# Optimization experiments

Hardware: AMD Instinct MI355X
Metric: run time of the kernel (lower is better)

## Reference

```python
import jax, jax.numpy as jnp
import numpy as np

FEAT_DIM = 1024
NUM_HEADS = 16
HEAD_DIM = FEAT_DIM // NUM_HEADS
B, T = 8, 1024


def setup_inputs() -> dict:
    key = jax.random.key(0)
    k_x, k_wqkv, k_bqkv, k_wp, k_bp = jax.random.split(key, 5)
    s = 1.0 / np.sqrt(FEAT_DIM)
    return {
        "x": jax.random.normal(k_x, (B, T, FEAT_DIM), dtype=jnp.float32),
        "padding_mask": jnp.zeros((B, T), dtype=bool),  # True = padded position
        "W_qkv": jax.random.normal(k_wqkv, (3 * FEAT_DIM, FEAT_DIM), dtype=jnp.float32) * s,
        "b_qkv": jax.random.normal(k_bqkv, (3 * FEAT_DIM,), dtype=jnp.float32) * 0.01,
        "W_proj": jax.random.normal(k_wp, (FEAT_DIM, FEAT_DIM), dtype=jnp.float32) * s,
        "b_proj": jax.random.normal(k_bp, (FEAT_DIM,), dtype=jnp.float32) * 0.01,
        "scale_factor": jnp.asarray(1.0 / np.sqrt(HEAD_DIM), dtype=jnp.float32),
    }


def reference(x, padding_mask, W_qkv, b_qkv, W_proj, b_proj, scale_factor):
    Bb, Tt, D = x.shape
    H, hd = NUM_HEADS, HEAD_DIM
    # fused QKV projection: [B,T,3D] -> [3,B,H,T,hd]
    qkv = (x @ W_qkv.T + b_qkv).reshape(Bb, Tt, 3, H, hd).transpose(2, 0, 3, 1, 4)
    q, k, v = qkv[0], qkv[1], qkv[2]
    # scores [B,H,T,T]
    attn = jnp.einsum("bhqd,bhkd->bhqk", q, k) * scale_factor
    causal = jnp.triu(jnp.ones((Tt, Tt), dtype=bool), k=1)  # [T,T]
    mask = causal[None, None] | padding_mask[:, None, None, :]  # [B,H,T,T] via broadcast
    attn = jnp.where(mask, -jnp.inf, attn)
    attn = jax.nn.softmax(attn, axis=-1)
    # dropout is identity in eval mode
    out = jnp.einsum("bhqk,bhkd->bqhd", attn, v).reshape(Bb, Tt, D)
    return out @ W_proj.T + b_proj
```

## Files before the change

### kernel.cpp

```cpp
#include <hip/hip_runtime.h>
#include <cstdint>
#include <cstddef>

typedef unsigned short u16;
typedef __attribute__((ext_vector_type(2))) unsigned short u16x2;
typedef __attribute__((ext_vector_type(4))) unsigned short u16x4;
typedef __attribute__((ext_vector_type(8))) unsigned short u16x8;
typedef __attribute__((ext_vector_type(8))) short s16x8;
typedef __attribute__((ext_vector_type(4))) float f32x4;

__device__ __forceinline__ u16 f2bf(float f) {
  uint32_t u = __float_as_uint(f);
  u += 0x7fffu + ((u >> 16) & 1u);
  return (u16)(u >> 16);
}

__device__ __forceinline__ f32x4 mfma16(s16x8 a, s16x8 b, f32x4 c) {
  return __builtin_amdgcn_mfma_f32_16x16x32_bf16(a, b, c, 0, 0, 0);
}

#define GLDS16(gp, lp) __builtin_amdgcn_global_load_lds(                     \
    (const __attribute__((address_space(1))) void*)(gp),                      \
    (__attribute__((address_space(3))) void*)(lp), 16, 0, 0)

__global__ void cvt_all(const float* __restrict__ x, const float* __restrict__ wq,
                        const float* __restrict__ wp, u16* __restrict__ xb,
                        u16* __restrict__ wqb, u16* __restrict__ wpb) {
  const int n4x = 2097152, n4q = 786432, n4p = 262144;
  const int total = n4x + n4q + n4p;
  const int stride = gridDim.x * blockDim.x;
  for (int i = blockIdx.x * blockDim.x + threadIdx.x; i < total; i += stride) {
    const float* src;
    u16* dst;
    int j = i;
    if (j < n4x) {
      src = x; dst = xb;
    } else if (j < n4x + n4q) {
      j -= n4x; src = wq; dst = wqb;
    } else {
      j -= n4x + n4q; src = wp; dst = wpb;
    }
    f32x4 v = ((const f32x4*)src)[j];
    u16x4 o;
    o[0] = f2bf(v[0]); o[1] = f2bf(v[1]); o[2] = f2bf(v[2]); o[3] = f2bf(v[3]);
    ((u16x4*)dst)[j] = o;
  }
}

template <int OUT_BF16>
__global__ __launch_bounds__(256, 2)
void gemm_bt(const u16* __restrict__ A, const u16* __restrict__ B,
             const float* __restrict__ bias, u16* __restrict__ Cb,
             float* __restrict__ Cf, int M, int N, int K, int tilesN) {
  __shared__ u16 lA[128 * 32];
  __shared__ u16 lB[128 * 32];

  int bid = blockIdx.x;
  int cpx = gridDim.x >> 3;
  bid = (bid & 7) * cpx + (bid >> 3);

  const int tm = bid / tilesN, tn = bid % tilesN;
  const int row0 = tm * 128, col0 = tn * 128;
  const int tid = threadIdx.x;
  const int lane = tid & 63, wave = tid >> 6;

  const u16* Ag = A + (size_t)(row0 + (tid >> 2)) * K + (tid & 3) * 8;
  const u16* Bg = B + (size_t)(col0 + (tid >> 2)) * K + (tid & 3) * 8;
  const int ldsoff = tid * 8;

  const int wm = (wave >> 1) * 64, wn = (wave & 1) * 64;
  const int fr = lane & 15, fk = (lane >> 4) * 8;

  f32x4 acc[4][4] = {};

  for (int k0 = 0; k0 < K; k0 += 32) {
    __syncthreads();
    GLDS16(Ag + k0, &lA[ldsoff]);
    GLDS16(Ag + (size_t)64 * K + k0, &lA[2048 + ldsoff]);
    GLDS16(Bg + k0, &lB[ldsoff]);
    GLDS16(Bg + (size_t)64 * K + k0, &lB[2048 + ldsoff]);
    __syncthreads();

    s16x8 af[4], bfr[4];
#pragma unroll
    for (int i = 0; i < 4; ++i) af[i] = *(const s16x8*)&lA[(wm + i * 16 + fr) * 32 + fk];
#pragma unroll
    for (int i = 0; i < 4; ++i) bfr[i] = *(const s16x8*)&lB[(wn + i * 16 + fr) * 32 + fk];
#pragma unroll
    for (int i = 0; i < 4; ++i)
#pragma unroll
      for (int j = 0; j < 4; ++j) acc[i][j] = mfma16(af[i], bfr[j], acc[i][j]);
  }

#pragma unroll
  for (int i = 0; i < 4; ++i) {
#pragma unroll
    for (int r = 0; r < 4; ++r) {
      const int row = row0 + wm + i * 16 + (lane >> 4) * 4 + r;
#pragma unroll
      for (int j = 0; j < 4; ++j) {
        const int col = col0 + wn + j * 16 + fr;
        const float v = acc[i][j][r] + bias[col];
        if (OUT_BF16)
          Cb[(size_t)row * N + col] = f2bf(v);
        else
          Cf[(size_t)row * N + col] = v;
      }
    }
  }
}

__global__ __launch_bounds__(256)
void vtrans(const u16* __restrict__ qkv, u16* __restrict__ vt) {
  __shared__ u16 lT[64][68];
  const int bid = blockIdx.x;
  const int bh = bid >> 4;
  const int tt = bid & 15;
  const int b = bh >> 4, h = bh & 15;
  const int tid = threadIdx.x;
  const int row = tid >> 2;
  const int cc = (tid & 3) * 16;

  const u16* src = qkv + (size_t)(b * 1024 + tt * 64 + row) * 3072 + 2048 + h * 64 + cc;
  *(u16x8*)&lT[row][cc] = *(const u16x8*)src;
  *(u16x8*)&lT[row][cc + 8] = *(const u16x8*)(src + 8);
  __syncthreads();

  u16 tmp[16];
#pragma unroll
  for (int i = 0; i < 16; ++i) tmp[i] = lT[cc + i][row];
  u16* dst = vt + (size_t)(bh * 64 + row) * 1024 + tt * 64 + cc;
  *(u16x8*)dst = *(u16x8*)&tmp[0];
  *(u16x8*)(dst + 8) = *(u16x8*)&tmp[8];
}

template <int NF, bool CAUSAL>
__device__ __forceinline__ void attn_step(
    const u16* __restrict__ Kbase, const u16* __restrict__ Vbase,
    const float* __restrict__ pb, u16* __restrict__ lp, int kvb, int qb,
    int fr, int grp, const s16x8 qf[2][2], f32x4 oacc[2][4], float m2[2],
    float l2[2], float cs) {
  f32x4 st[NF][2];
#pragma unroll
  for (int f = 0; f < NF; ++f) {
    const u16* kp = Kbase + (size_t)(kvb + f * 16 + fr) * 3072 + grp * 8;
    s16x8 ka0 = *(const s16x8*)kp;
    s16x8 ka1 = *(const s16x8*)(kp + 32);
    f32x4 a0 = {0.f, 0.f, 0.f, 0.f}, a1 = {0.f, 0.f, 0.f, 0.f};
    a0 = mfma16(ka0, qf[0][0], a0);
    a0 = mfma16(ka1, qf[0][1], a0);
    a1 = mfma16(ka0, qf[1][0], a1);
    a1 = mfma16(ka1, qf[1][1], a1);
    st[f][0] = a0;
    st[f][1] = a1;
  }

  f32x4 pbv[NF];
#pragma unroll
  for (int f = 0; f < NF; ++f)
    pbv[f] = *(const f32x4*)&pb[kvb + f * 16 + grp * 4];

  float tm[2];
#pragma unroll
  for (int g = 0; g < 2; ++g) {
    const int q = qb + g * 16 + fr;
    float t = -3.0e38f;
#pragma unroll
    for (int f = 0; f < NF; ++f)
#pragma unroll
      for (int r = 0; r < 4; ++r) {
        float v = __builtin_fmaf(st[f][g][r], cs, pbv[f][r]);
        if (CAUSAL) {
          const int kv = kvb + f * 16 + grp * 4 + r;
          v = (kv > q) ? -3.0e38f : v;
        }
        st[f][g][r] = v;
        t = fmaxf(t, v);
      }
    t = fmaxf(t, __shfl_xor(t, 16));
    t = fmaxf(t, __shfl_xor(t, 32));
    tm[g] = t;
  }

  const bool defer = __all((tm[0] <= m2[0] + 8.0f) && (tm[1] <= m2[1] + 8.0f)) != 0;
  if (!defer) {
#pragma unroll
    for (int g = 0; g < 2; ++g) {
      const float mn = fmaxf(m2[g], tm[g]);
      const float al = __expf(m2[g] - mn);
      m2[g] = mn;
      l2[g] *= al;
      float ar[4];
#pragma unroll
      for (int r = 0; r < 4; ++r) ar[r] = __shfl(al, grp * 4 + r);
#pragma unroll
      for (int nf = 0; nf < 4; ++nf) {
        oacc[g][nf][0] *= ar[0];
        oacc[g][nf][1] *= ar[1];
        oacc[g][nf][2] *= ar[2];
        oacc[g][nf][3] *= ar[3];
      }
    }
  }

#pragma unroll
  for (int g = 0; g < 2; ++g) {
    float rsum = 0.f;
#pragma unroll
    for (int f = 0; f < NF; ++f)
#pragma unroll
      for (int rp = 0; rp < 2; ++rp) {
        const float p0 = __expf(st[f][g][2 * rp] - m2[g]);
        const float p1 = __expf(st[f][g][2 * rp + 1] - m2[g]);
        rsum += p0 + p1;
        const uint32_t pk = __builtin_amdgcn_perm(
            __float_as_uint(p1) + 0x8000u, __float_as_uint(p0) + 0x8000u,
            0x07060302u);
        *(uint32_t*)&lp[(g * 16 + fr) * 72 + f * 16 + grp * 4 + 2 * rp] = pk;
      }
    rsum += __shfl_xor(rsum, 16);
    rsum += __shfl_xor(rsum, 32);
    l2[g] += rsum;
  }

  s16x8 pa[2][NF / 2];
#pragma unroll
  for (int g = 0; g < 2; ++g)
#pragma unroll
    for (int kc = 0; kc < NF / 2; ++kc)
      pa[g][kc] = *(const s16x8*)&lp[(g * 16 + fr) * 72 + kc * 32 + grp * 8];
#pragma unroll
  for (int nf = 0; nf < 4; ++nf) {
    const u16* vp = Vbase + (size_t)(nf * 16 + fr) * 1024 + kvb + grp * 8;
    s16x8 vb0 = *(const s16x8*)vp;
#pragma unroll
    for (int g = 0; g < 2; ++g) {
      f32x4 o = oacc[g][nf];
      o = mfma16(pa[g][0], vb0, o);
      if (NF == 4) o = mfma16(pa[g][1], *(const s16x8*)(vp + 32), o);
      oacc[g][nf] = o;
    }
  }
}

__global__ __launch_bounds__(256)
void attn3(const u16* __restrict__ qkv, const u16* __restrict__ vt,
           const unsigned char* __restrict__ pmask,
           const float* __restrict__ scale_ptr, u16* __restrict__ outp) {
  __shared__ u16 lP[4][32 * 72];
  __shared__ float lPb[1024];
  const int tid = threadIdx.x;
  const int lane = tid & 63, wave = tid >> 6;
  const int fr = lane & 15, grp = lane >> 4;
  const int w = blockIdx.x * 4 + wave;
  const int qc = 31 - (w >> 7);
  const int bh = w & 127;
  const int b = bh >> 4, h = bh & 15;
  const int qb = qc * 32;
  const float cs = scale_ptr[0];

  for (int i = tid; i < 1024; i += 256)
    lPb[i] = pmask[b * 1024 + i] ? -3.0e38f : 0.0f;
  __syncthreads();

  const u16* Kbase = qkv + (size_t)b * 1024 * 3072 + 1024 + h * 64;
  const u16* Vbase = vt + (size_t)bh * 64 * 1024;
  u16* lp = &lP[wave][0];

  s16x8 qf[2][2];
#pragma unroll
  for (int g = 0; g < 2; ++g)
#pragma unroll
    for (int c = 0; c < 2; ++c)
      qf[g][c] = *(const s16x8*)(qkv + (size_t)(b * 1024 + qb + g * 16 + fr) * 3072 +
                                 h * 64 + c * 32 + grp * 8);

  f32x4 oacc[2][4] = {};
  float m2[2] = {-1e30f, -1e30f};
  float l2[2] = {0.0f, 0.0f};

  const int FT = qc >> 1;
  for (int t = 0; t < FT; ++t)
    attn_step<4, false>(Kbase, Vbase, lPb, lp, t * 64, qb, fr, grp, qf, oacc, m2, l2, cs);
  if (qc & 1)
    attn_step<2, false>(Kbase, Vbase, lPb, lp, qb - 32, qb, fr, grp, qf, oacc, m2, l2, cs);
  attn_step<2, true>(Kbase, Vbase, lPb, lp, qb, qb, fr, grp, qf, oacc, m2, l2, cs);

#pragma unroll
  for (int g = 0; g < 2; ++g) {
    float linv[4];
#pragma unroll
    for (int r = 0; r < 4; ++r) linv[r] = 1.0f / __shfl(l2[g], grp * 4 + r);
#pragma unroll
    for (int nf = 0; nf < 4; ++nf)
#pragma unroll
      for (int r = 0; r < 4; ++r) {
        const int tq = qb + g * 16 + grp * 4 + r;
        outp[(size_t)(b * 1024 + tq) * 1024 + h * 64 + nf * 16 + fr] =
            f2bf(oacc[g][nf][r] * linv[r]);
      }
  }
}

extern "C" void kernel_launch(void* const* d_in, const int* in_sizes, int n_in,
                              void* d_out, int out_size, void* d_ws, size_t ws_size,
                              hipStream_t stream) {
  const float* x = (const float*)d_in[0];
  const unsigned char* pmask = (const unsigned char*)d_in[1];
  const float* Wqkv = (const float*)d_in[2];
  const float* bqkv = (const float*)d_in[3];
  const float* Wproj = (const float*)d_in[4];
  const float* bproj = (const float*)d_in[5];
  const float* scale = (const float*)d_in[6];
  float* out = (float*)d_out;

  char* ws = (char*)d_ws;
  u16* xb     = (u16*)(ws + 0);
  u16* vtb    = (u16*)(ws + 0);
  u16* wqkvb  = (u16*)(ws + 16777216);
  u16* wprojb = (u16*)(ws + 23068672);
  u16* qkv    = (u16*)(ws + 25165824);
  u16* attno  = (u16*)(ws + 75497472);
  if (ws_size < (size_t)92274688) return;

  cvt_all<<<2048, 256, 0, stream>>>(x, Wqkv, Wproj, xb, wqkvb, wprojb);

  gemm_bt<1><<<64 * 24, 256, 0, stream>>>(xb, wqkvb, bqkv, qkv, nullptr,
                                          8192, 3072, 1024, 24);
  vtrans<<<2048, 256, 0, stream>>>(qkv, vtb);
  attn3<<<1024, 256, 0, stream>>>(qkv, vtb, pmask, scale, attno);
  gemm_bt<0><<<64 * 8, 256, 0, stream>>>(attno, wprojb, bproj, nullptr, out,
                                         8192, 1024, 1024, 8);
}
```

Before: 266.7 us.

## Shrink attention per-wave query tile to 16 rows and double wave count

The attention kernel now gives each wave 16 query rows instead of 32, launches twice as many blocks, and adds a launch bound of 8 blocks per CU. Register and LDS use per wave drop, which should raise occupancy and give a finer causal-triangle load balance. The cost is that every K/V fragment is now loaded from global memory twice as often per query row, because each wave reuses it across only 16 rows, and the MFMA work per load is halved.

```diff
diff --git a/kernel.cpp b/kernel.cpp
--- a/kernel.cpp
+++ b/kernel.cpp
@@ -135,24 +135,21 @@
 }
 
 template <int NF, bool CAUSAL>
-__device__ __forceinline__ void attn_step(
+__device__ __forceinline__ void attn_step5(
     const u16* __restrict__ Kbase, const u16* __restrict__ Vbase,
     const float* __restrict__ pb, u16* __restrict__ lp, int kvb, int qb,
-    int fr, int grp, const s16x8 qf[2][2], f32x4 oacc[2][4], float m2[2],
-    float l2[2], float cs) {
-  f32x4 st[NF][2];
+    int fr, int grp, const s16x8 qf[2], f32x4 oacc[4], float& m2, float& l2,
+    float cs) {
+  f32x4 st[NF];
 #pragma unroll
   for (int f = 0; f < NF; ++f) {
     const u16* kp = Kbase + (size_t)(kvb + f * 16 + fr) * 3072 + grp * 8;
     s16x8 ka0 = *(const s16x8*)kp;
     s16x8 ka1 = *(const s16x8*)(kp + 32);
-    f32x4 a0 = {0.f, 0.f, 0.f, 0.f}, a1 = {0.f, 0.f, 0.f, 0.f};
-    a0 = mfma16(ka0, qf[0][0], a0);
-    a0 = mfma16(ka1, qf[0][1], a0);
-    a1 = mfma16(ka0, qf[1][0], a1);
-    a1 = mfma16(ka1, qf[1][1], a1);
-    st[f][0] = a0;
-    st[f][1] = a1;
+    f32x4 a = {0.f, 0.f, 0.f, 0.f};
+    a = mfma16(ka0, qf[0], a);
+    a = mfma16(ka1, qf[1], a);
+    st[f] = a;
   }
 
   f32x4 pbv[NF];
@@ -160,103 +157,86 @@
   for (int f = 0; f < NF; ++f)
     pbv[f] = *(const f32x4*)&pb[kvb + f * 16 + grp * 4];
 
-  float tm[2];
-#pragma unroll
-  for (int g = 0; g < 2; ++g) {
-    const int q = qb + g * 16 + fr;
-    float t = -3.0e38f;
-#pragma unroll
-    for (int f = 0; f < NF; ++f)
-#pragma unroll
-      for (int r = 0; r < 4; ++r) {
-        float v = __builtin_fmaf(st[f][g][r], cs, pbv[f][r]);
-        if (CAUSAL) {
-          const int kv = kvb + f * 16 + grp * 4 + r;
-          v = (kv > q) ? -3.0e38f : v;
-        }
-        st[f][g][r] = v;
-        t = fmaxf(t, v);
+  const int q = qb + fr;
+  float t = -3.0e38f;
+#pragma unroll
+  for (int f = 0; f < NF; ++f)
+#pragma unroll
+    for (int r = 0; r < 4; ++r) {
+      float v = __builtin_fmaf(st[f][r], cs, pbv[f][r]);
+      if (CAUSAL) {
+        const int kv = kvb + f * 16 + grp * 4 + r;
+        v = (kv > q) ? -3.0e38f : v;
       }
-    t = fmaxf(t, __shfl_xor(t, 16));
-    t = fmaxf(t, __shfl_xor(t, 32));
-    tm[g] = t;
-  }
-
-  const bool defer = __all((tm[0] <= m2[0] + 8.0f) && (tm[1] <= m2[1] + 8.0f)) != 0;
-  if (!defer) {
-#pragma unroll
-    for (int g = 0; g < 2; ++g) {
-      const float mn = fmaxf(m2[g], tm[g]);
-      const float al = __expf(m2[g] - mn);
-      m2[g] = mn;
-      l2[g] *= al;
-      float ar[4];
-#pragma unroll
-      for (int r = 0; r < 4; ++r) ar[r] = __shfl(al, grp * 4 + r);
-#pragma unroll
-      for (int nf = 0; nf < 4; ++nf) {
-        oacc[g][nf][0] *= ar[0];
-        oacc[g][nf][1] *= ar[1];
-        oacc[g][nf][2] *= ar[2];
-        oacc[g][nf][3] *= ar[3];
-      }
-    }
-  }
-
-#pragma unroll
-  for (int g = 0; g < 2; ++g) {
-    float rsum = 0.f;
-#pragma unroll
-    for (int f = 0; f < NF; ++f)
-#pragma unroll
-      for (int rp = 0; rp < 2; ++rp) {
-        const float p0 = __expf(st[f][g][2 * rp] - m2[g]);
-        const float p1 = __expf(st[f][g][2 * rp + 1] - m2[g]);
-        rsum += p0 + p1;
-        const uint32_t pk = __builtin_amdgcn_perm(
-            __float_as_uint(p1) + 0x8000u, __float_as_uint(p0) + 0x8000u,
-            0x07060302u);
-        *(uint32_t*)&lp[(g * 16 + fr) * 72 + f * 16 + grp * 4 + 2 * rp] = pk;
-      }
-    rsum += __shfl_xor(rsum, 16);
-    rsum += __shfl_xor(rsum, 32);
-    l2[g] += rsum;
-  }
-
-  s16x8 pa[2][NF / 2];
-#pragma unroll
-  for (int g = 0; g < 2; ++g)
-#pragma unroll
-    for (int kc = 0; kc < NF / 2; ++kc)
-      pa[g][kc] = *(const s16x8*)&lp[(g * 16 + fr) * 72 + kc * 32 + grp * 8];
+      st[f][r] = v;
+      t = fmaxf(t, v);
+    }
+  t = fmaxf(t, __shfl_xor(t, 16));
+  t = fmaxf(t, __shfl_xor(t, 32));
+
+  if (!__all(t <= m2 + 8.0f)) {
+    const float mn = fmaxf(m2, t);
+    const float al = __expf(m2 - mn);
+    m2 = mn;
+    l2 *= al;
+    float ar[4];
+#pragma unroll
+    for (int r = 0; r < 4; ++r) ar[r] = __shfl(al, grp * 4 + r);
+#pragma unroll
+    for (int nf = 0; nf < 4; ++nf) {
+      oacc[nf][0] *= ar[0];
+      oacc[nf][1] *= ar[1];
+      oacc[nf][2] *= ar[2];
+      oacc[nf][3] *= ar[3];
+    }
+  }
+
+  float rsum = 0.f;
+#pragma unroll
+  for (int f = 0; f < NF; ++f)
+#pragma unroll
+    for (int rp = 0; rp < 2; ++rp) {
+      const float p0 = __expf(st[f][2 * rp] - m2);
+      const float p1 = __expf(st[f][2 * rp + 1] - m2);
+      rsum += p0 + p1;
+      const uint32_t pk = __builtin_amdgcn_perm(
+          __float_as_uint(p1) + 0x8000u, __float_as_uint(p0) + 0x8000u,
+          0x07060302u);
+      *(uint32_t*)&lp[fr * 72 + f * 16 + grp * 4 + 2 * rp] = pk;
+    }
+  rsum += __shfl_xor(rsum, 16);
+  rsum += __shfl_xor(rsum, 32);
+  l2 += rsum;
+
+  s16x8 pa[NF / 2];
+#pragma unroll
+  for (int kc = 0; kc < NF / 2; ++kc)
+    pa[kc] = *(const s16x8*)&lp[fr * 72 + kc * 32 + grp * 8];
 #pragma unroll
   for (int nf = 0; nf < 4; ++nf) {
     const u16* vp = Vbase + (size_t)(nf * 16 + fr) * 1024 + kvb + grp * 8;
     s16x8 vb0 = *(const s16x8*)vp;
-#pragma unroll
-    for (int g = 0; g < 2; ++g) {
-      f32x4 o = oacc[g][nf];
-      o = mfma16(pa[g][0], vb0, o);
-      if (NF == 4) o = mfma16(pa[g][1], *(const s16x8*)(vp + 32), o);
-      oacc[g][nf] = o;
-    }
-  }
-}
-
-__global__ __launch_bounds__(256)
-void attn3(const u16* __restrict__ qkv, const u16* __restrict__ vt,
+    f32x4 o = oacc[nf];
+    o = mfma16(pa[0], vb0, o);
+    if (NF == 4) o = mfma16(pa[1], *(const s16x8*)(vp + 32), o);
+    oacc[nf] = o;
+  }
+}
+
+__global__ __launch_bounds__(256, 8)
+void attn5(const u16* __restrict__ qkv, const u16* __restrict__ vt,
            const unsigned char* __restrict__ pmask,
            const float* __restrict__ scale_ptr, u16* __restrict__ outp) {
-  __shared__ u16 lP[4][32 * 72];
+  __shared__ u16 lP[4][16 * 72];
   __shared__ float lPb[1024];
   const int tid = threadIdx.x;
   const int lane = tid & 63, wave = tid >> 6;
   const int fr = lane & 15, grp = lane >> 4;
   const int w = blockIdx.x * 4 + wave;
-  const int qc = 31 - (w >> 7);
+  const int qi = 63 - (w >> 7);
   const int bh = w & 127;
   const int b = bh >> 4, h = bh & 15;
-  const int qb = qc * 32;
+  const int qb = qi * 16;
   const float cs = scale_ptr[0];
 
   for (int i = tid; i < 1024; i += 256)
@@ -267,39 +247,34 @@
   const u16* Vbase = vt + (size_t)bh * 64 * 1024;
   u16* lp = &lP[wave][0];
 
-  s16x8 qf[2][2];
-#pragma unroll
-  for (int g = 0; g < 2; ++g)
-#pragma unroll
-    for (int c = 0; c < 2; ++c)
-      qf[g][c] = *(const s16x8*)(qkv + (size_t)(b * 1024 + qb + g * 16 + fr) * 3072 +
-                                 h * 64 + c * 32 + grp * 8);
-
-  f32x4 oacc[2][4] = {};
-  float m2[2] = {-1e30f, -1e30f};
-  float l2[2] = {0.0f, 0.0f};
-
-  const int FT = qc >> 1;
-  for (int t = 0; t < FT; ++t)
-    attn_step<4, false>(Kbase, Vbase, lPb, lp, t * 64, qb, fr, grp, qf, oacc, m2, l2, cs);
-  if (qc & 1)
-    attn_step<2, false>(Kbase, Vbase, lPb, lp, qb - 32, qb, fr, grp, qf, oacc, m2, l2, cs);
-  attn_step<2, true>(Kbase, Vbase, lPb, lp, qb, qb, fr, grp, qf, oacc, m2, l2, cs);
-
-#pragma unroll
-  for (int g = 0; g < 2; ++g) {
-    float linv[4];
-#pragma unroll
-    for (int r = 0; r < 4; ++r) linv[r] = 1.0f / __shfl(l2[g], grp * 4 + r);
-#pragma unroll
-    for (int nf = 0; nf < 4; ++nf)
-#pragma unroll
-      for (int r = 0; r < 4; ++r) {
-        const int tq = qb + g * 16 + grp * 4 + r;
-        outp[(size_t)(b * 1024 + tq) * 1024 + h * 64 + nf * 16 + fr] =
-            f2bf(oacc[g][nf][r] * linv[r]);
-      }
-  }
+  s16x8 qf[2];
+#pragma unroll
+  for (int c = 0; c < 2; ++c)
+    qf[c] = *(const s16x8*)(qkv + (size_t)(b * 1024 + qb + fr) * 3072 +
+                            h * 64 + c * 32 + grp * 8);
+
+  f32x4 oacc[4] = {};
+  float m2 = -1e30f, l2 = 0.0f;
+
+  const int n = qi >> 1;
+  int u = 0;
+  for (; u + 2 <= n; u += 2)
+    attn_step5<4, false>(Kbase, Vbase, lPb, lp, u * 32, qb, fr, grp, qf, oacc, m2, l2, cs);
+  if (u < n)
+    attn_step5<2, false>(Kbase, Vbase, lPb, lp, u * 32, qb, fr, grp, qf, oacc, m2, l2, cs);
+  attn_step5<2, true>(Kbase, Vbase, lPb, lp, n * 32, qb, fr, grp, qf, oacc, m2, l2, cs);
+
+  float linv[4];
+#pragma unroll
+  for (int r = 0; r < 4; ++r) linv[r] = 1.0f / __shfl(l2, grp * 4 + r);
+#pragma unroll
+  for (int nf = 0; nf < 4; ++nf)
+#pragma unroll
+    for (int r = 0; r < 4; ++r) {
+      const int tq = qb + grp * 4 + r;
+      outp[(size_t)(b * 1024 + tq) * 1024 + h * 64 + nf * 16 + fr] =
+          f2bf(oacc[nf][r] * linv[r]);
+    }
 }
 
 extern "C" void kernel_launch(void* const* d_in, const int* in_sizes, int n_in,
@@ -328,7 +303,7 @@
   gemm_bt<1><<<64 * 24, 256, 0, stream>>>(xb, wqkvb, bqkv, qkv, nullptr,
                                           8192, 3072, 1024, 24);
   vtrans<<<2048, 256, 0, stream>>>(qkv, vtb);
-  attn3<<<1024, 256, 0, stream>>>(qkv, vtb, pmask, scale, attno);
+  attn5<<<2048, 256, 0, stream>>>(qkv, vtb, pmask, scale, attno);
   gemm_bt<0><<<64 * 8, 256, 0, stream>>>(attno, wprojb, bproj, nullptr, out,
                                          8192, 1024, 1024, 8);
 }
```

Measured after the change: 364.3 us. 1.37x slower.

## Pair low and high causal query tiles per wave to balance attention work

Applied to the files above, without the earlier changes.

Each wave now processes two 16-row query tiles, one from the start and its mirror from the end of the sequence, so every wave does about the same amount of causal work instead of the old 32-row contiguous blocks of very different length. The key/value loop first runs both tiles together up to the low tile's diagonal, then continues with only the high tile, with the MFMAs, masking and softmax skipped for the inactive tile. Rescale deferral is now decided per tile, and launch bounds ask for 4 blocks per CU. The cost is that K/V fragments loaded in the shared phase feed only 16-row MFMAs, and the template has more variants, which may raise register use.

```diff
diff --git a/kernel.cpp b/kernel.cpp
--- a/kernel.cpp
+++ b/kernel.cpp
@@ -134,25 +134,30 @@
   *(u16x8*)(dst + 8) = *(u16x8*)&tmp[8];
 }
 
-template <int NF, bool CAUSAL>
-__device__ __forceinline__ void attn_step(
+template <int NF, bool LO, bool HI, bool CLO, bool CHI>
+__device__ __forceinline__ void attn_step6(
     const u16* __restrict__ Kbase, const u16* __restrict__ Vbase,
-    const float* __restrict__ pb, u16* __restrict__ lp, int kvb, int qb,
-    int fr, int grp, const s16x8 qf[2][2], f32x4 oacc[2][4], float m2[2],
-    float l2[2], float cs) {
+    const float* __restrict__ pb, u16* __restrict__ lp, int kvb, int qblo,
+    int qbhi, int fr, int grp, const s16x8 qf[2][2], f32x4 oacc[2][4],
+    float m2[2], float l2[2], float cs) {
   f32x4 st[NF][2];
 #pragma unroll
   for (int f = 0; f < NF; ++f) {
     const u16* kp = Kbase + (size_t)(kvb + f * 16 + fr) * 3072 + grp * 8;
     s16x8 ka0 = *(const s16x8*)kp;
     s16x8 ka1 = *(const s16x8*)(kp + 32);
-    f32x4 a0 = {0.f, 0.f, 0.f, 0.f}, a1 = {0.f, 0.f, 0.f, 0.f};
-    a0 = mfma16(ka0, qf[0][0], a0);
-    a0 = mfma16(ka1, qf[0][1], a0);
-    a1 = mfma16(ka0, qf[1][0], a1);
-    a1 = mfma16(ka1, qf[1][1], a1);
-    st[f][0] = a0;
-    st[f][1] = a1;
+    if (LO) {
+      f32x4 a = {0.f, 0.f, 0.f, 0.f};
+      a = mfma16(ka0, qf[0][0], a);
+      a = mfma16(ka1, qf[0][1], a);
+      st[f][0] = a;
+    }
+    if (HI) {
+      f32x4 a = {0.f, 0.f, 0.f, 0.f};
+      a = mfma16(ka0, qf[1][0], a);
+      a = mfma16(ka1, qf[1][1], a);
+      st[f][1] = a;
+    }
   }
 
   f32x4 pbv[NF];
@@ -160,17 +165,18 @@
   for (int f = 0; f < NF; ++f)
     pbv[f] = *(const f32x4*)&pb[kvb + f * 16 + grp * 4];
 
-  float tm[2];
 #pragma unroll
   for (int g = 0; g < 2; ++g) {
-    const int q = qb + g * 16 + fr;
+    if ((g == 0 && !LO) || (g == 1 && !HI)) continue;
+    const bool CG = (g == 0) ? CLO : CHI;
+    const int q = ((g == 0) ? qblo : qbhi) + fr;
     float t = -3.0e38f;
 #pragma unroll
     for (int f = 0; f < NF; ++f)
 #pragma unroll
       for (int r = 0; r < 4; ++r) {
         float v = __builtin_fmaf(st[f][g][r], cs, pbv[f][r]);
-        if (CAUSAL) {
+        if (CG) {
           const int kv = kvb + f * 16 + grp * 4 + r;
           v = (kv > q) ? -3.0e38f : v;
         }
@@ -179,14 +185,9 @@
       }
     t = fmaxf(t, __shfl_xor(t, 16));
     t = fmaxf(t, __shfl_xor(t, 32));
-    tm[g] = t;
-  }
-
-  const bool defer = __all((tm[0] <= m2[0] + 8.0f) && (tm[1] <= m2[1] + 8.0f)) != 0;
-  if (!defer) {
-#pragma unroll
-    for (int g = 0; g < 2; ++g) {
-      const float mn = fmaxf(m2[g], tm[g]);
+
+    if (!__all(t <= m2[g] + 8.0f)) {
+      const float mn = fmaxf(m2[g], t);
       const float al = __expf(m2[g] - mn);
       m2[g] = mn;
       l2[g] *= al;
@@ -201,10 +202,7 @@
         oacc[g][nf][3] *= ar[3];
       }
     }
-  }
-
-#pragma unroll
-  for (int g = 0; g < 2; ++g) {
+
     float rsum = 0.f;
 #pragma unroll
     for (int f = 0; f < NF; ++f)
@@ -225,26 +223,31 @@
 
   s16x8 pa[2][NF / 2];
 #pragma unroll
-  for (int g = 0; g < 2; ++g)
+  for (int g = 0; g < 2; ++g) {
+    if ((g == 0 && !LO) || (g == 1 && !HI)) continue;
 #pragma unroll
     for (int kc = 0; kc < NF / 2; ++kc)
       pa[g][kc] = *(const s16x8*)&lp[(g * 16 + fr) * 72 + kc * 32 + grp * 8];
+  }
 #pragma unroll
   for (int nf = 0; nf < 4; ++nf) {
     const u16* vp = Vbase + (size_t)(nf * 16 + fr) * 1024 + kvb + grp * 8;
     s16x8 vb0 = *(const s16x8*)vp;
+    s16x8 vb1;
+    if (NF == 4) vb1 = *(const s16x8*)(vp + 32);
 #pragma unroll
     for (int g = 0; g < 2; ++g) {
+      if ((g == 0 && !LO) || (g == 1 && !HI)) continue;
       f32x4 o = oacc[g][nf];
       o = mfma16(pa[g][0], vb0, o);
-      if (NF == 4) o = mfma16(pa[g][1], *(const s16x8*)(vp + 32), o);
+      if (NF == 4) o = mfma16(pa[g][1], vb1, o);
       oacc[g][nf] = o;
     }
   }
 }
 
-__global__ __launch_bounds__(256)
-void attn3(const u16* __restrict__ qkv, const u16* __restrict__ vt,
+__global__ __launch_bounds__(256, 4)
+void attn6(const u16* __restrict__ qkv, const u16* __restrict__ vt,
            const unsigned char* __restrict__ pmask,
            const float* __restrict__ scale_ptr, u16* __restrict__ outp) {
   __shared__ u16 lP[4][32 * 72];
@@ -252,11 +255,12 @@
   const int tid = threadIdx.x;
   const int lane = tid & 63, wave = tid >> 6;
   const int fr = lane & 15, grp = lane >> 4;
-  const int w = blockIdx.x * 4 + wave;
-  const int qc = 31 - (w >> 7);
-  const int bh = w & 127;
+  const int bid = blockIdx.x;
+  const int bh = bid & 127;
   const int b = bh >> 4, h = bh & 15;
-  const int qb = qc * 32;
+  const int p = (bid >> 7) * 4 + wave;
+  const int qblo = p * 16;
+  const int qbhi = (63 - p) * 16;
   const float cs = scale_ptr[0];
 
   for (int i = tid; i < 1024; i += 256)
@@ -269,25 +273,47 @@
 
   s16x8 qf[2][2];
 #pragma unroll
-  for (int g = 0; g < 2; ++g)
+  for (int g = 0; g < 2; ++g) {
+    const int qb = g ? qbhi : qblo;
 #pragma unroll
     for (int c = 0; c < 2; ++c)
-      qf[g][c] = *(const s16x8*)(qkv + (size_t)(b * 1024 + qb + g * 16 + fr) * 3072 +
+      qf[g][c] = *(const s16x8*)(qkv + (size_t)(b * 1024 + qb + fr) * 3072 +
                                  h * 64 + c * 32 + grp * 8);
+  }
 
   f32x4 oacc[2][4] = {};
   float m2[2] = {-1e30f, -1e30f};
   float l2[2] = {0.0f, 0.0f};
 
-  const int FT = qc >> 1;
-  for (int t = 0; t < FT; ++t)
-    attn_step<4, false>(Kbase, Vbase, lPb, lp, t * 64, qb, fr, grp, qf, oacc, m2, l2, cs);
-  if (qc & 1)
-    attn_step<2, false>(Kbase, Vbase, lPb, lp, qb - 32, qb, fr, grp, qf, oacc, m2, l2, cs);
-  attn_step<2, true>(Kbase, Vbase, lPb, lp, qb, qb, fr, grp, qf, oacc, m2, l2, cs);
+  const int nlo = (p >> 1) + 1;
+  const int nhi = ((63 - p) >> 1) + 1;
+
+  int u = 0;
+  for (; u + 2 <= nlo - 1; u += 2)
+    attn_step6<4, true, true, false, false>(Kbase, Vbase, lPb, lp, u * 32,
+                                            qblo, qbhi, fr, grp, qf, oacc, m2, l2, cs);
+  if (u < nlo - 1) {
+    attn_step6<2, true, true, false, false>(Kbase, Vbase, lPb, lp, u * 32,
+                                            qblo, qbhi, fr, grp, qf, oacc, m2, l2, cs);
+    ++u;
+  }
+  attn_step6<2, true, true, true, false>(Kbase, Vbase, lPb, lp, (nlo - 1) * 32,
+                                         qblo, qbhi, fr, grp, qf, oacc, m2, l2, cs);
+  u = nlo;
+  for (; u + 2 <= nhi - 1; u += 2)
+    attn_step6<4, false, true, false, false>(Kbase, Vbase, lPb, lp, u * 32,
+                                             qblo, qbhi, fr, grp, qf, oacc, m2, l2, cs);
+  if (u < nhi - 1) {
+    attn_step6<2, false, true, false, false>(Kbase, Vbase, lPb, lp, u * 32,
+                                             qblo, qbhi, fr, grp, qf, oacc, m2, l2, cs);
+    ++u;
+  }
+  attn_step6<2, false, true, false, true>(Kbase, Vbase, lPb, lp, (nhi - 1) * 32,
+                                          qblo, qbhi, fr, grp, qf, oacc, m2, l2, cs);
 
 #pragma unroll
   for (int g = 0; g < 2; ++g) {
+    const int qb = g ? qbhi : qblo;
     float linv[4];
 #pragma unroll
     for (int r = 0; r < 4; ++r) linv[r] = 1.0f / __shfl(l2[g], grp * 4 + r);
@@ -295,7 +321,7 @@
     for (int nf = 0; nf < 4; ++nf)
 #pragma unroll
       for (int r = 0; r < 4; ++r) {
-        const int tq = qb + g * 16 + grp * 4 + r;
+        const int tq = qb + grp * 4 + r;
         outp[(size_t)(b * 1024 + tq) * 1024 + h * 64 + nf * 16 + fr] =
             f2bf(oacc[g][nf][r] * linv[r]);
       }
@@ -328,7 +354,7 @@
   gemm_bt<1><<<64 * 24, 256, 0, stream>>>(xb, wqkvb, bqkv, qkv, nullptr,
                                           8192, 3072, 1024, 24);
   vtrans<<<2048, 256, 0, stream>>>(qkv, vtb);
-  attn3<<<1024, 256, 0, stream>>>(qkv, vtb, pmask, scale, attno);
+  attn6<<<1024, 256, 0, stream>>>(qkv, vtb, pmask, scale, attno);
   gemm_bt<0><<<64 * 8, 256, 0, stream>>>(attno, wprojb, bproj, nullptr, out,
                                          8192, 1024, 1024, 8);
 }
```

After: 296.3 us. 11.1% more time.
